# Optimization experiments

Hardware: AMD Instinct MI355X
Metric: run time of the kernel (lower is better)

Reference implementation:

```python
import jax, jax.numpy as jnp
import numpy as np

DMIN, DMAX = -1.0, 1.0
B, I, O, K = 1024, 256, 256, 128

def setup_inputs() -> dict:
    key = jax.random.key(0)
    k1, k2, k3 = jax.random.split(key, 3)
    x = jax.random.normal(k1, (B, I), dtype=jnp.float32)
    bound = 1.0 / np.sqrt(I)
    base_weight = jax.random.uniform(k2, (O, I), dtype=jnp.float32, minval=-bound, maxval=bound)
    coeff = 0.03 * jax.random.normal(k3, (O, I, K), dtype=jnp.float32)
    coeff = coeff - coeff.mean(axis=-1, keepdims=True)
    return {
        'x': x,
        'base_weight': base_weight,
        'spline_coefficients': coeff,
        'spline_scale': jnp.ones((O, I), dtype=jnp.float32),
        'bias': jnp.zeros((O,), dtype=jnp.float32),
    }


def reference(x, base_weight, spline_coefficients, spline_scale, bias):
    num_knots = spline_coefficients.shape[-1]
    step = (DMAX - DMIN) / (num_knots - 1)
    # input activation (tanh) then clamp to spline domain
    p = jnp.tanh(x)                                   # (B, I)
    c = jnp.clip(p, DMIN, DMAX)
    scaled = (c - DMIN) / step                        # in [0, K-1]
    left = jnp.clip(jnp.floor(scaled).astype(jnp.int32), 0, num_knots - 1)
    right = jnp.minimum(left + 1, num_knots - 1)
    frac = scaled - left.astype(p.dtype)              # (B, I)
    # fold spline_scale into coefficients, then gather only the 2 relevant knots
    Cs = spline_coefficients * spline_scale[..., None]  # (O, I, K)
    ii = jnp.arange(x.shape[1])[None, :]                # (1, I) broadcasts with (B, I)
    cl = Cs[:, ii, left]                                # (O, B, I)
    cr = Cs[:, ii, right]                               # (O, B, I)
    spline = jnp.einsum('bi,obi->bo', 1.0 - frac, cl) + jnp.einsum('bi,obi->bo', frac, cr)
    base = jax.nn.silu(p) @ base_weight.T               # (B, O)
    return base + spline + bias[None, :]
```

## Files before the change

kernel.cpp:

```cpp
#include <hip/hip_runtime.h>

constexpr int Bb = 1024;
constexpr int Ii = 256;
constexpr int Oo = 256;
constexpr int Kk = 128;
constexpr int NCH = 8;

typedef unsigned short u16;
typedef unsigned int u32;
typedef u16 ushort4v __attribute__((ext_vector_type(4)));

__device__ __forceinline__ float bf16u_to_f(u16 u) {
    union { u32 ui; float f; } c;
    c.ui = ((u32)u) << 16;
    return c.f;
}
__device__ __forceinline__ u16 f_to_bf16(float f) {
    union { float f; u32 u; } c; c.f = f;
    u32 r = c.u + 0x7fffu + ((c.u >> 16) & 1u);
    return (u16)(r >> 16);
}

__global__ __launch_bounds__(256) void kperm(const float* __restrict__ cs,
                                             const float* __restrict__ scale,
                                             const float* __restrict__ wbase,
                                             u16* __restrict__ cp,
                                             float* __restrict__ wt) {
    __shared__ u16 T[128 * 66];
    int blk = blockIdx.x;
    int chunk = blk & 7;
    int sub = blk >> 3;
    int i  = chunk * 32 + (sub & 31);
    int oh = (sub >> 5) & 1, kh = (sub >> 6) & 1;
    int o0 = oh << 7, kb = kh << 6;
    int t = threadIdx.x;

    {
        int c4 = t & 15;
        int rb = t >> 4;
        const float4* cs4 = (const float4*)cs;
#pragma unroll
        for (int p = 0; p < 8; ++p) {
            int r = p * 16 + rb;
            int o = o0 + r;
            float sc = scale[o * Ii + i];
            float4 val = cs4[(size_t)(o * Ii + i) * (Kk / 4) + kh * 16 + c4];
            int kl = c4 * 4;
            T[r * 66 + kl + 0] = f_to_bf16(val.x * sc);
            T[r * 66 + kl + 1] = f_to_bf16(val.y * sc);
            T[r * 66 + kl + 2] = f_to_bf16(val.z * sc);
            T[r * 66 + kl + 3] = f_to_bf16(val.w * sc);
        }
    }
    __syncthreads();
    {
        int og = t & 63;
        int kg = t >> 6;
#pragma unroll
        for (int m = 0; m < 16; ++m) {
            int kl = kg * 16 + m;
            u32 lo = T[(og * 2) * 66 + kl];
            u32 hi = T[(og * 2 + 1) * 66 + kl];
            *(u32*)&cp[((size_t)i * Kk + kb + kl) * Oo + o0 + og * 2] = lo | (hi << 16);
        }
    }
    if (blk < 256) {
        int gid = blk * 256 + t;
        wt[gid] = wbase[(gid & 255) * Ii + (gid >> 8)];
    }
}

__global__ __launch_bounds__(256, 8) void kmain(const float* __restrict__ x,
                                                const char* __restrict__ cpb,
                                                const float* __restrict__ wt,
                                                float4* __restrict__ part4) {
    __shared__ float4 sf[128];
    __shared__ float wbuf[8 * 256];
    int t = threadIdx.x;
    int blk = blockIdx.x;
    int chunk = blk & (NCH - 1);
    int b0 = (blk >> 3) << 2;
    int i0 = chunk << 5;

    if (t < 128) {
        int il = t >> 2, bl = t & 3;
        float xv = x[(size_t)(b0 + bl) * Ii + i0 + il];
        float e2 = __expf(2.f * xv);
        float p = 1.f - 2.f / (e2 + 1.f);
        float s = p / (1.f + __expf(-p));
        float c = fminf(fmaxf(p, -1.f), 1.f);
        float scaled = (c + 1.f) * ((float)(Kk - 1) * 0.5f);
        int l = (int)floorf(scaled);
        l = min(max(l, 0), Kk - 1);
        int rr = min(l + 1, Kk - 1);
        float4 v;
        v.x = scaled - (float)l;
        v.y = s;
        v.z = __int_as_float(l * (Oo * 2));
        v.w = __int_as_float(rr * (Oo * 2));
        sf[t] = v;
    }

    int oq = t & 63;
    int bh = t >> 6;

    float a0 = 0.f, a1 = 0.f, a2 = 0.f, a3 = 0.f;
    const char* cbase = cpb + (size_t)i0 * (Kk * Oo * 2) + oq * 8;

#pragma unroll
    for (int jb = 0; jb < 4; ++jb) {
        __syncthreads();
        {
            const float* wsrc = wt + (size_t)(i0 + jb * 8) * Oo;
#pragma unroll
            for (int p = 0; p < 8; ++p)
                wbuf[t + p * 256] = wsrc[t + p * 256];
        }
        __syncthreads();
#pragma unroll
        for (int m = 0; m < 8; ++m) {
            int il = jb * 8 + m;
            float4 v = sf[il * 4 + bh];
            float4 w = *(const float4*)&wbuf[m * 256 + oq * 4];
            const char* ci = cbase + (size_t)il * (Kk * Oo * 2);
            ushort4v cl = *(const ushort4v*)(ci + __float_as_int(v.z));
            ushort4v cr = *(const ushort4v*)(ci + __float_as_int(v.w));
            float f = v.x, g = 1.f - v.x, s = v.y;
            a0 = fmaf(s, w.x, a0);
            a1 = fmaf(s, w.y, a1);
            a2 = fmaf(s, w.z, a2);
            a3 = fmaf(s, w.w, a3);
            a0 = fmaf(g, bf16u_to_f(cl.x), a0);
            a1 = fmaf(g, bf16u_to_f(cl.y), a1);
            a2 = fmaf(g, bf16u_to_f(cl.z), a2);
            a3 = fmaf(g, bf16u_to_f(cl.w), a3);
            a0 = fmaf(f, bf16u_to_f(cr.x), a0);
            a1 = fmaf(f, bf16u_to_f(cr.y), a1);
            a2 = fmaf(f, bf16u_to_f(cr.z), a2);
            a3 = fmaf(f, bf16u_to_f(cr.w), a3);
        }
    }
    float4 r; r.x = a0; r.y = a1; r.z = a2; r.w = a3;
    part4[(size_t)chunk * (Bb * Oo / 4) + (size_t)(b0 + bh) * (Oo / 4) + oq] = r;
}

__global__ __launch_bounds__(256) void kreduce(const float4* __restrict__ part4,
                                               const float4* __restrict__ bias4,
                                               float4* __restrict__ out4) {
    int gid = blockIdx.x * 256 + threadIdx.x;
    const float4* p = part4 + gid;
    float4 s = p[0];
#pragma unroll
    for (int c = 1; c < NCH; ++c) {
        float4 v = p[(size_t)c * (Bb * Oo / 4)];
        s.x += v.x; s.y += v.y; s.z += v.z; s.w += v.w;
    }
    float4 bv = bias4[gid & 63];
    s.x += bv.x; s.y += bv.y; s.z += bv.z; s.w += bv.w;
    out4[gid] = s;
}

extern "C" void kernel_launch(void* const* d_in, const int* in_sizes, int n_in,
                              void* d_out, int out_size, void* d_ws, size_t ws_size,
                              hipStream_t stream) {
    const float* x     = (const float*)d_in[0];
    const float* wbase = (const float*)d_in[1];
    const float* coeff = (const float*)d_in[2];
    const float* scale = (const float*)d_in[3];
    const float* bias  = (const float*)d_in[4];
    float* out = (float*)d_out;

    char* ws = (char*)d_ws;
    u16*    cp    = (u16*)ws;
    float*  wt    = (float*)(ws + (16u << 20));
    float4* part4 = (float4*)(ws + (17u << 20));

    kperm<<<1024, 256, 0, stream>>>(coeff, scale, wbase, cp, wt);
    kmain<<<2048, 256, 0, stream>>>(x, (const char*)cp, wt, part4);
    kreduce<<<(Bb * Oo / 4) / 256, 256, 0, stream>>>(part4, (const float4*)bias, (float4*)out);
}
```

Measured before the change: 109.4 us.

## Compute two batch rows per thread in kmain to reuse weight loads

Each kmain block now covers 8 batch rows instead of 4, so each thread accumulates two rows against the same base-weight float4 from shared memory. The grid is halved, launch bounds drop to 4 blocks per SM, and the inner loop unroll is reduced to 4. This spreads the LDS weight staging and its barriers over more work. In exchange it raises register pressure and lowers occupancy, and the coefficient gathers, which are random per row, still scale with the batch.

```diff
diff --git a/kernel.cpp b/kernel.cpp
--- a/kernel.cpp
+++ b/kernel.cpp
@@ -70,20 +70,20 @@
     }
 }
 
-__global__ __launch_bounds__(256, 8) void kmain(const float* __restrict__ x,
+__global__ __launch_bounds__(256, 4) void kmain(const float* __restrict__ x,
                                                 const char* __restrict__ cpb,
                                                 const float* __restrict__ wt,
                                                 float4* __restrict__ part4) {
-    __shared__ float4 sf[128];
+    __shared__ float4 sf[256];
     __shared__ float wbuf[8 * 256];
     int t = threadIdx.x;
     int blk = blockIdx.x;
     int chunk = blk & (NCH - 1);
-    int b0 = (blk >> 3) << 2;
+    int b0 = (blk >> 3) << 3;
     int i0 = chunk << 5;
 
-    if (t < 128) {
-        int il = t >> 2, bl = t & 3;
+    {
+        int il = t & 31, bl = t >> 5;
         float xv = x[(size_t)(b0 + bl) * Ii + i0 + il];
         float e2 = __expf(2.f * xv);
         float p = 1.f - 2.f / (e2 + 1.f);
@@ -98,13 +98,14 @@
         v.y = s;
         v.z = __int_as_float(l * (Oo * 2));
         v.w = __int_as_float(rr * (Oo * 2));
-        sf[t] = v;
+        sf[il * 8 + bl] = v;
     }
 
     int oq = t & 63;
-    int bh = t >> 6;
+    int bq = t >> 6;
 
-    float a0 = 0.f, a1 = 0.f, a2 = 0.f, a3 = 0.f;
+    float a00=0.f,a01=0.f,a02=0.f,a03=0.f;
+    float a10=0.f,a11=0.f,a12=0.f,a13=0.f;
     const char* cbase = cpb + (size_t)i0 * (Kk * Oo * 2) + oq * 8;
 
 #pragma unroll
@@ -117,31 +118,38 @@
                 wbuf[t + p * 256] = wsrc[t + p * 256];
         }
         __syncthreads();
-#pragma unroll
+#pragma unroll 4
         for (int m = 0; m < 8; ++m) {
             int il = jb * 8 + m;
-            float4 v = sf[il * 4 + bh];
+            float4 v0 = sf[il * 8 + bq * 2];
+            float4 v1 = sf[il * 8 + bq * 2 + 1];
             float4 w = *(const float4*)&wbuf[m * 256 + oq * 4];
             const char* ci = cbase + (size_t)il * (Kk * Oo * 2);
-            ushort4v cl = *(const ushort4v*)(ci + __float_as_int(v.z));
-            ushort4v cr = *(const ushort4v*)(ci + __float_as_int(v.w));
-            float f = v.x, g = 1.f - v.x, s = v.y;
-            a0 = fmaf(s, w.x, a0);
-            a1 = fmaf(s, w.y, a1);
-            a2 = fmaf(s, w.z, a2);
-            a3 = fmaf(s, w.w, a3);
-            a0 = fmaf(g, bf16u_to_f(cl.x), a0);
-            a1 = fmaf(g, bf16u_to_f(cl.y), a1);
-            a2 = fmaf(g, bf16u_to_f(cl.z), a2);
-            a3 = fmaf(g, bf16u_to_f(cl.w), a3);
-            a0 = fmaf(f, bf16u_to_f(cr.x), a0);
-            a1 = fmaf(f, bf16u_to_f(cr.y), a1);
-            a2 = fmaf(f, bf16u_to_f(cr.z), a2);
-            a3 = fmaf(f, bf16u_to_f(cr.w), a3);
+            ushort4v cl0 = *(const ushort4v*)(ci + __float_as_int(v0.z));
+            ushort4v cr0 = *(const ushort4v*)(ci + __float_as_int(v0.w));
+            ushort4v cl1 = *(const ushort4v*)(ci + __float_as_int(v1.z));
+            ushort4v cr1 = *(const ushort4v*)(ci + __float_as_int(v1.w));
+            float f0 = v0.x, g0 = 1.f - v0.x, s0 = v0.y;
+            float f1 = v1.x, g1 = 1.f - v1.x, s1 = v1.y;
+            a00 = fmaf(s0, w.x, a00); a01 = fmaf(s0, w.y, a01);
+            a02 = fmaf(s0, w.z, a02); a03 = fmaf(s0, w.w, a03);
+            a10 = fmaf(s1, w.x, a10); a11 = fmaf(s1, w.y, a11);
+            a12 = fmaf(s1, w.z, a12); a13 = fmaf(s1, w.w, a13);
+            a00 = fmaf(g0, bf16u_to_f(cl0.x), a00); a00 = fmaf(f0, bf16u_to_f(cr0.x), a00);
+            a01 = fmaf(g0, bf16u_to_f(cl0.y), a01); a01 = fmaf(f0, bf16u_to_f(cr0.y), a01);
+            a02 = fmaf(g0, bf16u_to_f(cl0.z), a02); a02 = fmaf(f0, bf16u_to_f(cr0.z), a02);
+            a03 = fmaf(g0, bf16u_to_f(cl0.w), a03); a03 = fmaf(f0, bf16u_to_f(cr0.w), a03);
+            a10 = fmaf(g1, bf16u_to_f(cl1.x), a10); a10 = fmaf(f1, bf16u_to_f(cr1.x), a10);
+            a11 = fmaf(g1, bf16u_to_f(cl1.y), a11); a11 = fmaf(f1, bf16u_to_f(cr1.y), a11);
+            a12 = fmaf(g1, bf16u_to_f(cl1.z), a12); a12 = fmaf(f1, bf16u_to_f(cr1.z), a12);
+            a13 = fmaf(g1, bf16u_to_f(cl1.w), a13); a13 = fmaf(f1, bf16u_to_f(cr1.w), a13);
         }
     }
-    float4 r; r.x = a0; r.y = a1; r.z = a2; r.w = a3;
-    part4[(size_t)chunk * (Bb * Oo / 4) + (size_t)(b0 + bh) * (Oo / 4) + oq] = r;
+    size_t cstride = (size_t)(Bb * Oo / 4);
+    float4 r0; r0.x=a00; r0.y=a01; r0.z=a02; r0.w=a03;
+    float4 r1; r1.x=a10; r1.y=a11; r1.z=a12; r1.w=a13;
+    part4[chunk * cstride + (size_t)(b0 + bq * 2) * (Oo / 4) + oq] = r0;
+    part4[chunk * cstride + (size_t)(b0 + bq * 2 + 1) * (Oo / 4) + oq] = r1;
 }
 
 __global__ __launch_bounds__(256) void kreduce(const float4* __restrict__ part4,
@@ -176,6 +184,6 @@
     float4* part4 = (float4*)(ws + (17u << 20));
 
     kperm<<<1024, 256, 0, stream>>>(coeff, scale, wbase, cp, wt);
-    kmain<<<2048, 256, 0, stream>>>(x, (const char*)cp, wt, part4);
+    kmain<<<1024, 256, 0, stream>>>(x, (const char*)cp, wt, part4);
     kreduce<<<(Bb * Oo / 4) / 256, 256, 0, stream>>>(part4, (const float4*)bias, (float4*)out);
 }
```

After: 109.2 us, median of 2. Within noise of the previous version (-0.2%).
